# Kernel tuning notes

Hardware: AMD Instinct MI355X
Metric: run time of the kernel (lower is better)

The kernel has to match this reference:

```python
import jax, jax.numpy as jnp
import numpy as np

FEAT = 128
N_RBF = 20
CUTOFF = 5.0
NUM_CONV = 3
N_ATOMS = 8000
N_EDGES = 160000
N_MOLS = 100
EPS = 1e-15


def silu(x):
    return x * jax.nn.sigmoid(x)


def setup_inputs() -> dict:
    key = jax.random.key(0)
    ks = jax.random.split(key, 16)
    F = FEAT

    def w(k, shape, fan_in):
        return jax.random.normal(k, shape, dtype=jnp.float32) / np.sqrt(fan_in).astype(np.float32)

    nbr0 = jax.random.randint(ks[12], (N_EDGES,), 0, N_ATOMS)
    # avoid self-edges (would give zero distance)
    nbr1 = (nbr0 + 1 + jax.random.randint(ks[13], (N_EDGES,), 0, N_ATOMS - 1)) % N_ATOMS
    return {
        "xyz": jax.random.uniform(ks[0], (N_ATOMS, 3), dtype=jnp.float32) * 10.0,
        "emb_table": jax.random.normal(ks[1], (100, F), dtype=jnp.float32),
        "msg_w1": w(ks[2], (NUM_CONV, F, F), F),
        "msg_b1": jnp.zeros((NUM_CONV, F), jnp.float32),
        "msg_w2": w(ks[3], (NUM_CONV, F, 3 * F), F),
        "msg_b2": jnp.zeros((NUM_CONV, 3 * F), jnp.float32),
        "rbf_w": w(ks[4], (NUM_CONV, N_RBF, 3 * F), N_RBF),
        "rbf_b": jnp.zeros((NUM_CONV, 3 * F), jnp.float32),
        "upd_u": w(ks[5], (NUM_CONV, F, F), F),
        "upd_v": w(ks[6], (NUM_CONV, F, F), F),
        "upd_w1": w(ks[7], (NUM_CONV, 2 * F, F), 2 * F),
        "upd_b1": jnp.zeros((NUM_CONV, F), jnp.float32),
        "upd_w2": w(ks[8], (NUM_CONV, F, 3 * F), F),
        "upd_b2": jnp.zeros((NUM_CONV, 3 * F), jnp.float32),
        "ro_w1": w(ks[9], (F, F // 2), F),
        "ro_b1": jnp.zeros((F // 2,), jnp.float32),
        "ro_w2": w(ks[10], (F // 2, 1), F // 2),
        "ro_b2": jnp.zeros((1,), jnp.float32),
        "z": jax.random.randint(ks[11], (N_ATOMS,), 0, 100),
        "nbrs": jnp.stack([nbr0, nbr1], axis=1),
        "mol_idx": jnp.sort(jax.random.randint(ks[14], (N_ATOMS,), 0, N_MOLS)),
    }


def painn_forward(xyz, emb_table, msg_w1, msg_b1, msg_w2, msg_b2, rbf_w, rbf_b,
                  upd_u, upd_v, upd_w1, upd_b1, upd_w2, upd_b2,
                  ro_w1, ro_b1, ro_w2, ro_b2, z, nbrs, mol_idx):
    F = FEAT
    N = xyz.shape[0]
    # r_ij points from nbrs[:,0] (center i) to nbrs[:,1] (neighbor j)
    r_ij = xyz[nbrs[:, 1]] - xyz[nbrs[:, 0]]            # (E, 3)
    d = jnp.sqrt(jnp.sum(r_ij * r_ij, axis=-1))         # (E,)
    unit = r_ij / d[:, None]                            # (E, 3)
    # PaiNN sinc radial basis: sin(n*pi*d/cutoff)/d, n = 1..n_rbf
    n = jnp.arange(1, N_RBF + 1, dtype=jnp.float32)
    rbf = jnp.sin(n[None, :] * jnp.pi * d[:, None] / CUTOFF) / d[:, None]  # (E, n_rbf)
    # cosine cutoff envelope
    env = jnp.where(d <= CUTOFF, 0.5 * (jnp.cos(jnp.pi * d / CUTOFF) + 1.0), 0.0)

    s = emb_table[z]                                    # (N, F)
    v = jnp.zeros((N, F, 3), dtype=s.dtype)             # (N, F, 3)

    for i in range(NUM_CONV):
        # ---- message block ----
        phi = silu(s @ msg_w1[i] + msg_b1[i]) @ msg_w2[i] + msg_b2[i]   # (N, 3F)
        w_s = (rbf @ rbf_w[i] + rbf_b[i]) * env[:, None]                # (E, 3F)
        inv = (phi[nbrs[:, 1]] * w_s).reshape(-1, 3, F)                 # (E, 3, F)
        split0 = inv[:, 0, :][..., None]                                # (E, F, 1)
        split1 = inv[:, 1, :]                                           # (E, F)
        split2 = inv[:, 2, :][..., None]                                # (E, F, 1)
        dv_ij = split2 * unit[:, None, :] + split0 * v[nbrs[:, 1]]      # (E, F, 3)
        ds = jax.ops.segment_sum(split1, nbrs[:, 0], num_segments=N)
        dv = jax.ops.segment_sum(dv_ij, nbrs[:, 0], num_segments=N)
        s = s + ds
        v = v + dv
        # ---- update block ----
        u_v = jnp.einsum('nfd,fg->ngd', v, upd_u[i])                    # (N, F, 3)
        v_v = jnp.einsum('nfd,fg->ngd', v, upd_v[i])                    # (N, F, 3)
        v_v_norm = jnp.sqrt(jnp.sum(v_v * v_v, axis=-1) + EPS)          # (N, F)
        stack = jnp.concatenate([s, v_v_norm], axis=-1)                 # (N, 2F)
        a = (silu(stack @ upd_w1[i] + upd_b1[i]) @ upd_w2[i] + upd_b2[i]).reshape(-1, 3, F)
        a_vv = a[:, 0, :][..., None]
        a_sv = a[:, 1, :]
        a_ss = a[:, 2, :]
        dv_u = u_v * a_vv
        ds_u = jnp.sum(u_v * v_v, axis=-1) * a_sv + a_ss
        s = s + ds_u
        v = v + dv_u

    # readout MLP + per-molecule sum pool (SumPool)
    atom_e = silu(s @ ro_w1 + ro_b1) @ ro_w2 + ro_b2                    # (N, 1)
    energy = jax.ops.segment_sum(atom_e, mol_idx, num_segments=N_MOLS)  # (N_MOLS, 1)
    return energy


def reference(xyz, emb_table, msg_w1, msg_b1, msg_w2, msg_b2, rbf_w, rbf_b,
              upd_u, upd_v, upd_w1, upd_b1, upd_w2, upd_b2,
              ro_w1, ro_b1, ro_w2, ro_b2, z, nbrs, mol_idx):
    return painn_forward(xyz, emb_table, msg_w1, msg_b1, msg_w2, msg_b2, rbf_w, rbf_b,
                         upd_u, upd_v, upd_w1, upd_b1, upd_w2, upd_b2,
                         ro_w1, ro_b1, ro_w2, ro_b2, z, nbrs, mol_idx)
```

## Files before the change

kernel.cpp:

```cpp
#include <hip/hip_runtime.h>

static constexpr int F = 128;
static constexpr int N_RBF = 20;
static constexpr int N_ATOMS = 8000;
static constexpr int NP = 8064;
static constexpr int N_EDGES = 160000;
static constexpr int N_MOLS = 100;
static constexpr float CUTOFF = 5.0f;
static constexpr size_t NFC = (size_t)NP * F;
static constexpr int REC = 28;
#define PIF 3.14159265358979323846f

typedef __attribute__((ext_vector_type(8))) short bf16x8;
typedef __attribute__((ext_vector_type(4))) float f32x4;
typedef unsigned short ushort_t;
typedef unsigned int uint_t;

__device__ __forceinline__ float silu_f(float x) { return x / (1.f + __expf(-x)); }

__device__ __forceinline__ ushort_t f2bf(float x) {
    union { float f; uint_t u; } v; v.f = x;
    uint_t r = v.u + 0x7fffu + ((v.u >> 16) & 1u);
    return (ushort_t)(r >> 16);
}
// ... 46 lines not shown
        int idx = base + i;
        if (idx < N_ATOMS) { offsets[idx] = ex; ex += local[i]; }
    }
}

__global__ __launch_bounds__(256) void build_kernel(
    const float* __restrict__ xyz, const int* __restrict__ nbrs,
    const float* __restrict__ envb, const int* __restrict__ offsets,
    int* __restrict__ cursor, float* __restrict__ rec)
{
    int e = blockIdx.x * 256 + threadIdx.x;
    if (e >= N_EDGES) return;
    float ev = envb[e];
    if (ev <= 0.f) return;
    int i0 = nbrs[2*e+0], i1 = nbrs[2*e+1];
    float dx = xyz[3*i1+0] - xyz[3*i0+0];
    float dy = xyz[3*i1+1] - xyz[3*i0+1];
    float dz = xyz[3*i1+2] - xyz[3*i0+2];
    float d  = sqrtf(dx*dx + dy*dy + dz*dz);
    float inv = 1.f / d;
    int pos = offsets[i0] + atomicAdd(&cursor[i0], 1);
    float* r = rec + (size_t)pos * REC;
    r[0] = __int_as_float(i1);
    r[1] = ev;
    r[2] = dx*inv; r[3] = dy*inv; r[4] = dz*inv;
    float base = PIF*d/CUTOFF;
    float sc = inv * ev;
    #pragma unroll
    for (int k = 0; k < N_RBF; ++k)
        r[5 + k] = sinf((float)(k+1)*base) * sc;
}

static constexpr int WPREP_W = 557056;
static constexpr int WPREP_TOTAL = 557184;
static constexpr int NATF = N_ATOMS * F;
static constexpr int PREP_TOTAL = NATF + WPREP_TOTAL + 2 * N_ATOMS;
__global__ __launch_bounds__(256) void prep_kernel(
    const float* __restrict__ emb, const int* __restrict__ z, float* __restrict__ s,
    const float* __restrict__ msg_w1, const float* __restrict__ msg_w2,
    const float* __restrict__ upd_u,  const float* __restrict__ upd_v,
    const float* __restrict__ upd_w1, const float* __restrict__ upd_w2,
    const float* __restrict__ ro_w1,  const float* __restrict__ ro_b1,
    ushort_t* __restrict__ dhi, ushort_t* __restrict__ dlo,
    float* __restrict__ robias, int* __restrict__ cntz)
{
    int gidx = blockIdx.x * 256 + threadIdx.x;
    if (gidx < NATF) {
        int n = gidx >> 7, f = gidx & 127;
        s[gidx] = emb[z[n]*F + f];
        return;
    }
    int idx = gidx - NATF;
    if (idx >= WPREP_TOTAL) {
        cntz[idx - WPREP_TOTAL] = 0;
        return;
    }
    if (idx >= WPREP_W) {
        int l = idx - WPREP_W;
        robias[l] = (l < 64) ? ro_b1[l] : 0.f;
        return;
    }
    float val;
    if (idx < 540672) {
        const float* src; int K, N, rem;
        if (idx < 49152)       { int l = idx;          int c = l / 16384; rem = l % 16384; K = 128; N = 128; src = msg_w1 + c * 16384; }
        else if (idx < 196608) { int l = idx - 49152;  int c = l / 49152; rem = l % 49152; K = 128; N = 384; src = msg_w2 + c * 49152; }
        else if (idx < 294912) { int l = idx - 196608; int c = l / 32768; rem = l % 32768; K = 128; N = 128;
                                 if (rem < 16384) src = upd_u + c * 16384;
                                 else { src = upd_v + c * 16384; rem -= 16384; } }
        else if (idx < 393216) { int l = idx - 294912; int c = l / 32768; rem = l % 32768; K = 256; N = 128; src = upd_w1 + c * 32768; }
        else                   { int l = idx - 393216; int c = l / 49152; rem = l % 49152; K = 128; N = 384; src = upd_w2 + c * 49152; }
        int n = rem / K, k = rem % K;
        val = src[k * N + n];
    } else {
        int l = idx - 540672;
        int n = l >> 7, k = l & 127;
        val = (n < 64) ? ro_w1[k * 64 + n] : 0.f;
    }
    ushort_t h = f2bf(val);
    dhi[idx] = h;
    dlo[idx] = f2bf(val - bf2f(h));
}

__global__ __launch_bounds__(256) void phi0_kernel(
    const float* __restrict__ sbuf,
    const ushort_t* __restrict__ W1h, const ushort_t* __restrict__ W1l,
    const float* __restrict__ b1,
    const ushort_t* __restrict__ W2h, const ushort_t* __restrict__ W2l,
    const float* __restrict__ b2,
    float* __restrict__ C)
{
    __shared__ __align__(16) ushort_t Ah[2][32 * 40], Al[2][32 * 40];
    __shared__ __align__(16) ushort_t Bh[2][128 * 40], Bl[2][128 * 40];
    __shared__ __align__(16) ushort_t Hh[32 * 136], Hl[32 * 136];
    const int tid = threadIdx.x;
    const int wave = tid >> 6, lane = tid & 63;
    const int row_l = lane & 15, quad = lane >> 4;
    const int wn = wave * 32;
    const int m0 = blockIdx.x * 32;
    const int lrA = tid >> 3, ksA = (tid & 7) * 4;
    const int lrB = tid >> 1, ksB = (tid & 1) * 16;

    float4 rx;
    uint4 b_h0, b_h1, b_l0, b_l1;

    auto loadB1 = [&](int k0) {
        const ushort_t* bh = &W1h[(size_t)lrB * 128 + k0 + ksB];
        const ushort_t* bl = &W1l[(size_t)lrB * 128 + k0 + ksB];
        b_h0 = *(const uint4*)bh; b_h1 = *(const uint4*)(bh + 8);
        b_l0 = *(const uint4*)bl; b_l1 = *(const uint4*)(bl + 8);
    };
    auto loadB2 = [&](int it2) {
        int ct = it2 >> 2, k0 = (it2 & 3) * 32;
        const ushort_t* bh = &W2h[(size_t)(ct * 128 + lrB) * 128 + k0 + ksB];
        const ushort_t* bl = &W2l[(size_t)(ct * 128 + lrB) * 128 + k0 + ksB];
        b_h0 = *(const uint4*)bh; b_h1 = *(const uint4*)(bh + 8);
        b_l0 = *(const uint4*)bl; b_l1 = *(const uint4*)(bl + 8);
    };
    auto writeA = [&](int buf) {
        float e[4] = {rx.x, rx.y, rx.z, rx.w};
        ushort_t ph[4], pl[4];
        #pragma unroll
        for (int t = 0; t < 4; ++t) {
            ushort_t h = f2bf(e[t]);
            ph[t] = h; pl[t] = f2bf(e[t] - bf2f(h));
        }
        *(uint2*)&Ah[buf][lrA * 40 + ksA] = *(uint2*)ph;
        *(uint2*)&Al[buf][lrA * 40 + ksA] = *(uint2*)pl;
    };
    auto writeB = [&](int buf) {
        *(uint4*)&Bh[buf][lrB * 40 + ksB]     = b_h0;
        *(uint4*)&Bh[buf][lrB * 40 + ksB + 8] = b_h1;
        *(uint4*)&Bl[buf][lrB * 40 + ksB]     = b_l0;
        *(uint4*)&Bl[buf][lrB * 40 + ksB + 8] = b_l1;
    };

    f32x4 acc[2][2];
    #pragma unroll
    for (int i = 0; i < 2; ++i)
        #pragma unroll
        for (int j = 0; j < 2; ++j)
            #pragma unroll
            for (int r = 0; r < 4; ++r) acc[i][j][r] = 0.f;

    rx = *(const float4*)&sbuf[(size_t)(m0 + lrA) * 128 + ksA];
    loadB1(0);
    writeA(0); writeB(0);
    __syncthreads();
    #pragma unroll
    for (int it = 0; it < 4; ++it) {
        const int k0n = (it + 1) * 32;
        if (it + 1 < 4) {
            rx = *(const float4*)&sbuf[(size_t)(m0 + lrA) * 128 + k0n + ksA];
            loadB1(k0n);
        }
        bf16x8 ahf[2], alf[2], bhf[2], blf[2];
        #pragma unroll
        for (int i = 0; i < 2; ++i) {
            int ar = (i * 16 + row_l) * 40 + quad * 8;
            ahf[i] = *(const bf16x8*)&Ah[it & 1][ar];
            alf[i] = *(const bf16x8*)&Al[it & 1][ar];
        }
        #pragma unroll
        for (int j = 0; j < 2; ++j) {
            int br = (wn + j * 16 + row_l) * 40 + quad * 8;
            bhf[j] = *(const bf16x8*)&Bh[it & 1][br];
            blf[j] = *(const bf16x8*)&Bl[it & 1][br];
        }
        #pragma unroll
        for (int i = 0; i < 2; ++i)
            #pragma unroll
            for (int j = 0; j < 2; ++j) {
                acc[i][j] = __builtin_amdgcn_mfma_f32_16x16x32_bf16(ahf[i], bhf[j], acc[i][j], 0, 0, 0);
                acc[i][j] = __builtin_amdgcn_mfma_f32_16x16x32_bf16(ahf[i], blf[j], acc[i][j], 0, 0, 0);
                acc[i][j] = __builtin_amdgcn_mfma_f32_16x16x32_bf16(alf[i], bhf[j], acc[i][j], 0, 0, 0);
            }
        if (it + 1 < 4) { writeA((it + 1) & 1); writeB((it + 1) & 1); }
        __syncthreads();
    }
    #pragma unroll
    for (int j = 0; j < 2; ++j) {
        int col = wn + j * 16 + row_l;
        float bval = b1[col];
        #pragma unroll
        for (int i = 0; i < 2; ++i)
            #pragma unroll
            for (int r = 0; r < 4; ++r) {
                int row = i * 16 + quad * 4 + r;
                float v = silu_f(acc[i][j][r] + bval);
                ushort_t h = f2bf(v);
                Hh[row * 136 + col] = h;
                Hl[row * 136 + col] = f2bf(v - bf2f(h));
            }
    }

    #pragma unroll
    for (int i = 0; i < 2; ++i)
        #pragma unroll
        for (int j = 0; j < 2; ++j)
            #pragma unroll
            for (int r = 0; r < 4; ++r) acc[i][j][r] = 0.f;
    loadB2(0); writeB(0);
    __syncthreads();
    #pragma unroll
    for (int it = 0; it < 12; ++it) {
        const int k0 = (it & 3) * 32;
        if (it + 1 < 12) loadB2(it + 1);
        bf16x8 ahf[2], alf[2], bhf[2], blf[2];
        #pragma unroll
        for (int i = 0; i < 2; ++i) {
            int ar = (i * 16 + row_l) * 136 + k0 + quad * 8;
            ahf[i] = *(const bf16x8*)&Hh[ar];
            alf[i] = *(const bf16x8*)&Hl[ar];
        }
        #pragma unroll
        for (int j = 0; j < 2; ++j) {
            int br = (wn + j * 16 + row_l) * 40 + quad * 8;
            bhf[j] = *(const bf16x8*)&Bh[it & 1][br];
            blf[j] = *(const bf16x8*)&Bl[it & 1][br];
        }
        #pragma unroll
        for (int i = 0; i < 2; ++i)
            #pragma unroll
            for (int j = 0; j < 2; ++j) {
                acc[i][j] = __builtin_amdgcn_mfma_f32_16x16x32_bf16(ahf[i], bhf[j], acc[i][j], 0, 0, 0);
                acc[i][j] = __builtin_amdgcn_mfma_f32_16x16x32_bf16(ahf[i], blf[j], acc[i][j], 0, 0, 0);
                acc[i][j] = __builtin_amdgcn_mfma_f32_16x16x32_bf16(alf[i], bhf[j], acc[i][j], 0, 0, 0);
            }
        if ((it & 3) == 3) {
            const int ct = it >> 2;
            #pragma unroll
            for (int j = 0; j < 2; ++j) {
                int col = ct * 128 + wn + j * 16 + row_l;
                float bval = b2[col];
                #pragma unroll
                for (int i = 0; i < 2; ++i)
                    #pragma unroll
                    for (int r = 0; r < 4; ++r) {
                        int row = i * 16 + quad * 4 + r;
                        C[(size_t)(m0 + row) * 384 + col] = acc[i][j][r] + bval;
                    }
            }
            #pragma unroll
            for (int i = 0; i < 2; ++i)
                #pragma unroll
                for (int j = 0; j < 2; ++j)
                    #pragma unroll
                    for (int r = 0; r < 4; ++r) acc[i][j][r] = 0.f;
        }
        if (it + 1 < 12) writeB((it + 1) & 1);
        __syncthreads();
    }
}

template<int TAIL>
__global__ __launch_bounds__(256) void updphi_kernel(
    float* __restrict__ s_io, float* __restrict__ v_io,
    const ushort_t* __restrict__ UVh, const ushort_t* __restrict__ UVl,
    const ushort_t* __restrict__ W1h, const ushort_t* __restrict__ W1l,
    const float* __restrict__ b1,
    const ushort_t* __restrict__ W2h, const ushort_t* __restrict__ W2l,
    const float* __restrict__ b2,
    const ushort_t* __restrict__ XW1h, const ushort_t* __restrict__ XW1l,
    const float* __restrict__ xb1,
    const ushort_t* __restrict__ XW2h, const ushort_t* __restrict__ XW2l,
    const float* __restrict__ xb2,
    float* __restrict__ phi_out,
    const float* __restrict__ w2ro, const float* __restrict__ b2ro,
    const int* __restrict__ mol, float* __restrict__ outp)
{
    __shared__ float uvv[96][261];
    __shared__ __align__(16) ushort_t Bh[2][128 * 40];
    __shared__ __align__(16) ushort_t Bl[2][128 * 40];
    __shared__ __align__(16) unsigned char AH[17408];
    __shared__ float molacc[128];
    __shared__ float redl[32][4];
    const int tid = threadIdx.x;
    const int wave = tid >> 6, lane = tid & 63;
    const int row_l = lane & 15, quad = lane >> 4;
    const int wn = wave * 32;
    const int m0 = blockIdx.x * 32;
    const int lrA = tid >> 3;
    const int ksA = (tid & 7) * 4;
    const int lrB = tid >> 1, ksB = (tid & 1) * 16;

    float* sS = &uvv[0][0];
    constexpr int SSTR = 132;

    {
        ushort_t* A0h = (ushort_t*)AH;
        ushort_t* A0l = A0h + 96 * 40;
        ushort_t* B0h = &Bh[0][0];
        ushort_t* B0l = &Bl[0][0];
        f32x4 acc0[6][4];
        #pragma unroll
        for (int i = 0; i < 6; ++i)
            #pragma unroll
            for (int j = 0; j < 4; ++j)
                #pragma unroll
                for (int r = 0; r < 4; ++r) acc0[i][j][r] = 0.f;
        for (int k0 = 0; k0 < 128; k0 += 32) {
            #pragma unroll
            for (int g = 0; g < 3; ++g) {
                int row = g * 32 + lrA;
                float4 v = *(const float4*)&v_io[(size_t)(m0 * 3 + row) * 128 + k0 + ksA];
                float e[4] = {v.x, v.y, v.z, v.w};
                ushort_t ph[4], pl[4];
                #pragma unroll
                for (int t = 0; t < 4; ++t) {
                    ushort_t h = f2bf(e[t]);
                    ph[t] = h; pl[t] = f2bf(e[t] - bf2f(h));
                }
                *(uint2*)&A0h[row * 40 + ksA] = *(uint2*)ph;
                *(uint2*)&A0l[row * 40 + ksA] = *(uint2*)pl;
            }
            {
                const ushort_t* bh = &UVh[(size_t)tid * 128 + k0];
                const ushort_t* bl = &UVl[(size_t)tid * 128 + k0];
                *(uint4*)&B0h[tid * 40 + 0]  = *(const uint4*)(bh + 0);
                *(uint4*)&B0h[tid * 40 + 8]  = *(const uint4*)(bh + 8);
                *(uint4*)&B0h[tid * 40 + 16] = *(const uint4*)(bh + 16);
                *(uint4*)&B0h[tid * 40 + 24] = *(const uint4*)(bh + 24);
                *(uint4*)&B0l[tid * 40 + 0]  = *(const uint4*)(bl + 0);
                *(uint4*)&B0l[tid * 40 + 8]  = *(const uint4*)(bl + 8);
                *(uint4*)&B0l[tid * 40 + 16] = *(const uint4*)(bl + 16);
                *(uint4*)&B0l[tid * 40 + 24] = *(const uint4*)(bl + 24);
            }
            __syncthreads();
            bf16x8 a0h[6], a0l[6], b0h[4], b0l[4];
            #pragma unroll
            for (int i = 0; i < 6; ++i) {
                int ar = (i * 16 + row_l) * 40 + quad * 8;
                a0h[i] = *(const bf16x8*)&A0h[ar];
                a0l[i] = *(const bf16x8*)&A0l[ar];
            }
            #pragma unroll
            for (int j = 0; j < 4; ++j) {
                int br = (wave * 64 + j * 16 + row_l) * 40 + quad * 8;
                b0h[j] = *(const bf16x8*)&B0h[br];
                b0l[j] = *(const bf16x8*)&B0l[br];
            }
            #pragma unroll
            for (int i = 0; i < 6; ++i)
                #pragma unroll
                for (int j = 0; j < 4; ++j) {
                    acc0[i][j] = __builtin_amdgcn_mfma_f32_16x16x32_bf16(a0h[i], b0h[j], acc0[i][j], 0, 0, 0);
                    acc0[i][j] = __builtin_amdgcn_mfma_f32_16x16x32_bf16(a0h[i], b0l[j], acc0[i][j], 0, 0, 0);
                    acc0[i][j] = __builtin_amdgcn_mfma_f32_16x16x32_bf16(a0l[i], b0h[j], acc0[i][j], 0, 0, 0);
                }
            __syncthreads();
        }
        #pragma unroll
        for (int i = 0; i < 6; ++i)
            #pragma unroll
            for (int j = 0; j < 4; ++j)
                #pragma unroll
                for (int r = 0; r < 4; ++r)
                    uvv[i * 16 + quad * 4 + r][wave * 64 + j * 16 + row_l] = acc0[i][j][r];
        __syncthreads();
    }

    ushort_t* Ah1 = (ushort_t*)AH;
    ushort_t* Al1 = Ah1 + 2 * 32 * 40;
    ushort_t* Hh  = (ushort_t*)AH;
    ushort_t* Hl  = Hh + 32 * 136;

    float4 rx;
    uint4 b_h0, b_h1, b_l0, b_l1;

    auto loadB1 = [&](int k0) {
        const ushort_t* bh = &W1h[(size_t)lrB * 256 + k0 + ksB];
        const ushort_t* bl = &W1l[(size_t)lrB * 256 + k0 + ksB];
        b_h0 = *(const uint4*)bh; b_h1 = *(const uint4*)(bh + 8);
        b_l0 = *(const uint4*)bl; b_l1 = *(const uint4*)(bl + 8);
    };
    auto writeB = [&](int buf) {
        *(uint4*)&Bh[buf][lrB * 40 + ksB]     = b_h0;
        *(uint4*)&Bh[buf][lrB * 40 + ksB + 8] = b_h1;
        *(uint4*)&Bl[buf][lrB * 40 + ksB]     = b_l0;
        *(uint4*)&Bl[buf][lrB * 40 + ksB + 8] = b_l1;
    };
    auto writeA1 = [&](int buf, int k0) {
        float e[4];
        if (k0 < 128) {
            e[0] = rx.x; e[1] = rx.y; e[2] = rx.z; e[3] = rx.w;
        } else {
            int f = k0 + ksA;
            #pragma unroll
            for (int t = 0; t < 4; ++t) {
                float x = uvv[lrA * 3 + 0][f + t];
                float y = uvv[lrA * 3 + 1][f + t];
                float z = uvv[lrA * 3 + 2][f + t];
                e[t] = sqrtf(x * x + y * y + z * z + 1e-15f);
            }
        }
        ushort_t ph[4], pl[4];
        #pragma unroll
        for (int t = 0; t < 4; ++t) {
            ushort_t h = f2bf(e[t]);
            ph[t] = h; pl[t] = f2bf(e[t] - bf2f(h));
        }
        *(uint2*)&Ah1[buf * 1280 + lrA * 40 + ksA] = *(uint2*)ph;
        *(uint2*)&Al1[buf * 1280 + lrA * 40 + ksA] = *(uint2*)pl;
    };

    f32x4 acc[2][2];
    #pragma unroll
    for (int i = 0; i < 2; ++i)
        #pragma unroll
        for (int j = 0; j < 2; ++j)
            #pragma unroll
            for (int r = 0; r < 4; ++r) acc[i][j][r] = 0.f;

    rx = *(const float4*)&s_io[(size_t)(m0 + lrA) * 128 + ksA];
    loadB1(0);
    writeA1(0, 0); writeB(0);
    __syncthreads();
    #pragma unroll
    for (int it = 0; it < 8; ++it) {
        const int k0n = (it + 1) * 32;
        if (it + 1 < 8) {
            if (k0n < 128) rx = *(const float4*)&s_io[(size_t)(m0 + lrA) * 128 + k0n + ksA];
            loadB1(k0n);
        }
        bf16x8 ahf[2], alf[2], bhf[2], blf[2];
        #pragma unroll
        for (int i = 0; i < 2; ++i) {
            int ar = (it & 1) * 1280 + (i * 16 + row_l) * 40 + quad * 8;
            ahf[i] = *(const bf16x8*)&Ah1[ar];
            alf[i] = *(const bf16x8*)&Al1[ar];
        }
        #pragma unroll
        for (int j = 0; j < 2; ++j) {
            int br = (wn + j * 16 + row_l) * 40 + quad * 8;
            bhf[j] = *(const bf16x8*)&Bh[it & 1][br];
            blf[j] = *(const bf16x8*)&Bl[it & 1][br];
        }
        #pragma unroll
        for (int i = 0; i < 2; ++i)
            #pragma unroll
            for (int j = 0; j < 2; ++j) {
                acc[i][j] = __builtin_amdgcn_mfma_f32_16x16x32_bf16(ahf[i], bhf[j], acc[i][j], 0, 0, 0);
                acc[i][j] = __builtin_amdgcn_mfma_f32_16x16x32_bf16(ahf[i], blf[j], acc[i][j], 0, 0, 0);
                acc[i][j] = __builtin_amdgcn_mfma_f32_16x16x32_bf16(alf[i], bhf[j], acc[i][j], 0, 0, 0);
            }
        if (it + 1 < 8) { writeA1((it + 1) & 1, k0n); writeB((it + 1) & 1); }
        __syncthreads();
    }
    #pragma unroll
    for (int j = 0; j < 2; ++j) {
        int col = wn + j * 16 + row_l;
        float bval = b1[col];
        #pragma unroll
        for (int i = 0; i < 2; ++i)
            #pragma unroll
            for (int r = 0; r < 4; ++r) {
                int row = i * 16 + quad * 4 + r;
                float v = silu_f(acc[i][j][r] + bval);
                ushort_t h = f2bf(v);
                Hh[row * 136 + col] = h;
                Hl[row * 136 + col] = f2bf(v - bf2f(h));
            }
    }

    constexpr int CT0 = TAIL ? 1 : 0;
    constexpr int NIT2 = (3 - CT0) * 4;
    auto loadB2 = [&](int it2) {
        int ct = CT0 + (it2 >> 2), k0 = (it2 & 3) * 32;
        const ushort_t* bh = &W2h[(size_t)(ct * 128 + lrB) * 128 + k0 + ksB];
        const ushort_t* bl = &W2l[(size_t)(ct * 128 + lrB) * 128 + k0 + ksB];
        b_h0 = *(const uint4*)bh; b_h1 = *(const uint4*)(bh + 8);
        b_l0 = *(const uint4*)bl; b_l1 = *(const uint4*)(bl + 8);
    };

    #pragma unroll
    for (int i = 0; i < 2; ++i)
        #pragma unroll
        for (int j = 0; j < 2; ++j)
            #pragma unroll
            for (int r = 0; r < 4; ++r) acc[i][j][r] = 0.f;
    f32x4 ssum[2][2];

    loadB2(0); writeB(0);
    __syncthreads();
    #pragma unroll
    for (int it = 0; it < NIT2; ++it) {
        const int k0 = (it & 3) * 32;
        if (it + 1 < NIT2) loadB2(it + 1);
        bf16x8 ahf[2], alf[2], bhf[2], blf[2];
        #pragma unroll
        for (int i = 0; i < 2; ++i) {
            int ar = (i * 16 + row_l) * 136 + k0 + quad * 8;
            ahf[i] = *(const bf16x8*)&Hh[ar];
            alf[i] = *(const bf16x8*)&Hl[ar];
        }
        #pragma unroll
        for (int j = 0; j < 2; ++j) {
            int br = (wn + j * 16 + row_l) * 40 + quad * 8;
            bhf[j] = *(const bf16x8*)&Bh[it & 1][br];
            blf[j] = *(const bf16x8*)&Bl[it & 1][br];
        }
        #pragma unroll
        for (int i = 0; i < 2; ++i)
            #pragma unroll
            for (int j = 0; j < 2; ++j) {
                acc[i][j] = __builtin_amdgcn_mfma_f32_16x16x32_bf16(ahf[i], bhf[j], acc[i][j], 0, 0, 0);
                acc[i][j] = __builtin_amdgcn_mfma_f32_16x16x32_bf16(ahf[i], blf[j], acc[i][j], 0, 0, 0);
                acc[i][j] = __builtin_amdgcn_mfma_f32_16x16x32_bf16(alf[i], bhf[j], acc[i][j], 0, 0, 0);
            }
        if ((it & 3) == 3) {
            const int ct = CT0 + (it >> 2);
            #pragma unroll
            for (int j = 0; j < 2; ++j) {
                int f = wn + j * 16 + row_l;
                float bval = b2[ct * 128 + f];
                #pragma unroll
                for (int i = 0; i < 2; ++i)
                    #pragma unroll
                    for (int r = 0; r < 4; ++r) {
                        int ln = i * 16 + quad * 4 + r;
                        float a = acc[i][j][r] + bval;
                        if (ct == 0) {
                            size_t vb = (size_t)(m0 + ln) * 3 * F + f;
                            v_io[vb]         += uvv[ln * 3 + 0][f] * a;
                            v_io[vb + F]     += uvv[ln * 3 + 1][f] * a;
                            v_io[vb + 2 * F] += uvv[ln * 3 + 2][f] * a;
                        } else if (ct == 1) {
                            float dot = uvv[ln * 3 + 0][f] * uvv[ln * 3 + 0][128 + f]
                                      + uvv[ln * 3 + 1][f] * uvv[ln * 3 + 1][128 + f]
                                      + uvv[ln * 3 + 2][f] * uvv[ln * 3 + 2][128 + f];
                            ssum[i][j][r] = dot * a;
                        } else {
                            float sv = s_io[(size_t)(m0 + ln) * F + f] + ssum[i][j][r] + a;
                            if constexpr (TAIL == 0) s_io[(size_t)(m0 + ln) * F + f] = sv;
                            sS[ln * SSTR + f] = sv;
                        }
                    }
            }
            #pragma unroll
            for (int i = 0; i < 2; ++i)
                #pragma unroll
                for (int j = 0; j < 2; ++j)
                    #pragma unroll
                    for (int r = 0; r < 4; ++r) acc[i][j][r] = 0.f;
        }
        if (it + 1 < NIT2) writeB((it + 1) & 1);
        __syncthreads();
    }

    if constexpr (TAIL == 1) { if (tid < 128) molacc[tid] = 0.f; }
    ushort_t* Ah3 = (ushort_t*)AH;
    ushort_t* Al3 = Ah3 + 2 * 1280;

    auto loadB31 = [&](int k0) {
        const ushort_t* bh = &XW1h[(size_t)lrB * 128 + k0 + ksB];
        const ushort_t* bl = &XW1l[(size_t)lrB * 128 + k0 + ksB];
        b_h0 = *(const uint4*)bh; b_h1 = *(const uint4*)(bh + 8);
        b_l0 = *(const uint4*)bl; b_l1 = *(const uint4*)(bl + 8);
    };
    auto writeA3 = [&](int buf, int k0) {
        float e[4];
        #pragma unroll
        for (int t = 0; t < 4; ++t) e[t] = sS[lrA * SSTR + k0 + ksA + t];
        ushort_t ph[4], pl[4];
        #pragma unroll
        for (int t = 0; t < 4; ++t) {
            ushort_t h = f2bf(e[t]);
            ph[t] = h; pl[t] = f2bf(e[t] - bf2f(h));
        }
        *(uint2*)&Ah3[buf * 1280 + lrA * 40 + ksA] = *(uint2*)ph;
        *(uint2*)&Al3[buf * 1280 + lrA * 40 + ksA] = *(uint2*)pl;
    };

    #pragma unroll
    for (int i = 0; i < 2; ++i)
        #pragma unroll
        for (int j = 0; j < 2; ++j)
            #pragma unroll
            for (int r = 0; r < 4; ++r) acc[i][j][r] = 0.f;

    loadB31(0);
    writeA3(0, 0); writeB(0);
    __syncthreads();
    #pragma unroll
    for (int it = 0; it < 4; ++it) {
        const int k0n = (it + 1) * 32;
        if (it + 1 < 4) loadB31(k0n);
        bf16x8 ahf[2], alf[2], bhf[2], blf[2];
        #pragma unroll
        for (int i = 0; i < 2; ++i) {
            int ar = (it & 1) * 1280 + (i * 16 + row_l) * 40 + quad * 8;
            ahf[i] = *(const bf16x8*)&Ah3[ar];
            alf[i] = *(const bf16x8*)&Al3[ar];
        }
        #pragma unroll
        for (int j = 0; j < 2; ++j) {
            int br = (wn + j * 16 + row_l) * 40 + quad * 8;
            bhf[j] = *(const bf16x8*)&Bh[it & 1][br];
            blf[j] = *(const bf16x8*)&Bl[it & 1][br];
        }
        #pragma unroll
        for (int i = 0; i < 2; ++i)
            #pragma unroll
            for (int j = 0; j < 2; ++j) {
                acc[i][j] = __builtin_amdgcn_mfma_f32_16x16x32_bf16(ahf[i], bhf[j], acc[i][j], 0, 0, 0);
                acc[i][j] = __builtin_amdgcn_mfma_f32_16x16x32_bf16(ahf[i], blf[j], acc[i][j], 0, 0, 0);
                acc[i][j] = __builtin_amdgcn_mfma_f32_16x16x32_bf16(alf[i], bhf[j], acc[i][j], 0, 0, 0);
            }
        if (it + 1 < 4) { writeA3((it + 1) & 1, k0n); writeB((it + 1) & 1); }
        __syncthreads();
    }

    if constexpr (TAIL == 0) {
        #pragma unroll
        for (int j = 0; j < 2; ++j) {
            int col = wn + j * 16 + row_l;
            float bval = xb1[col];
            #pragma unroll
            for (int i = 0; i < 2; ++i)
                #pragma unroll
                for (int r = 0; r < 4; ++r) {
                    int row = i * 16 + quad * 4 + r;
                    float v = silu_f(acc[i][j][r] + bval);
                    ushort_t h = f2bf(v);
                    Hh[row * 136 + col] = h;
                    Hl[row * 136 + col] = f2bf(v - bf2f(h));
                }
        }
        auto loadB32 = [&](int it2) {
            int ct = it2 >> 2, k0 = (it2 & 3) * 32;
            const ushort_t* bh = &XW2h[(size_t)(ct * 128 + lrB) * 128 + k0 + ksB];
            const ushort_t* bl = &XW2l[(size_t)(ct * 128 + lrB) * 128 + k0 + ksB];
            b_h0 = *(const uint4*)bh; b_h1 = *(const uint4*)(bh + 8);
            b_l0 = *(const uint4*)bl; b_l1 = *(const uint4*)(bl + 8);
        };
        #pragma unroll
        for (int i = 0; i < 2; ++i)
            #pragma unroll
            for (int j = 0; j < 2; ++j)
                #pragma unroll
                for (int r = 0; r < 4; ++r) acc[i][j][r] = 0.f;
        loadB32(0); writeB(0);
        __syncthreads();
        #pragma unroll
        for (int it = 0; it < 12; ++it) {
            const int k0 = (it & 3) * 32;
            if (it + 1 < 12) loadB32(it + 1);
            bf16x8 ahf[2], alf[2], bhf[2], blf[2];
            #pragma unroll
            for (int i = 0; i < 2; ++i) {
                int ar = (i * 16 + row_l) * 136 + k0 + quad * 8;
                ahf[i] = *(const bf16x8*)&Hh[ar];
                alf[i] = *(const bf16x8*)&Hl[ar];
            }
            #pragma unroll
            for (int j = 0; j < 2; ++j) {
                int br = (wn + j * 16 + row_l) * 40 + quad * 8;
                bhf[j] = *(const bf16x8*)&Bh[it & 1][br];
                blf[j] = *(const bf16x8*)&Bl[it & 1][br];
            }
            #pragma unroll
            for (int i = 0; i < 2; ++i)
                #pragma unroll
                for (int j = 0; j < 2; ++j) {
                    acc[i][j] = __builtin_amdgcn_mfma_f32_16x16x32_bf16(ahf[i], bhf[j], acc[i][j], 0, 0, 0);
                    acc[i][j] = __builtin_amdgcn_mfma_f32_16x16x32_bf16(ahf[i], blf[j], acc[i][j], 0, 0, 0);
                    acc[i][j] = __builtin_amdgcn_mfma_f32_16x16x32_bf16(alf[i], bhf[j], acc[i][j], 0, 0, 0);
                }
            if ((it & 3) == 3) {
                const int ct = it >> 2;
                #pragma unroll
                for (int j = 0; j < 2; ++j) {
                    int col = ct * 128 + wn + j * 16 + row_l;
                    float bval = xb2[col];
                    #pragma unroll
                    for (int i = 0; i < 2; ++i)
                        #pragma unroll
                        for (int r = 0; r < 4; ++r) {
                            int row = i * 16 + quad * 4 + r;
                            phi_out[(size_t)(m0 + row) * 384 + col] = acc[i][j][r] + bval;
                        }
                }
                #pragma unroll
                for (int i = 0; i < 2; ++i)
                    #pragma unroll
                    for (int j = 0; j < 2; ++j)
                        #pragma unroll
                        for (int r = 0; r < 4; ++r) acc[i][j][r] = 0.f;
            }
            if (it + 1 < 12) writeB((it + 1) & 1);
            __syncthreads();
        }
    } else {
        float part[2][4];
        #pragma unroll
        for (int i = 0; i < 2; ++i)
            #pragma unroll
            for (int r = 0; r < 4; ++r) part[i][r] = 0.f;
        #pragma unroll
        for (int j = 0; j < 2; ++j) {
            int col = wn + j * 16 + row_l;
            float bv = xb1[col];
            float wv = (col < 64) ? w2ro[col] : 0.f;
            #pragma unroll
            for (int i = 0; i < 2; ++i)
                #pragma unroll
                for (int r = 0; r < 4; ++r)
                    part[i][r] += silu_f(acc[i][j][r] + bv) * wv;
        }
        #pragma unroll
        for (int o = 1; o < 16; o <<= 1)
            #pragma unroll
            for (int i = 0; i < 2; ++i)
                #pragma unroll
                for (int r = 0; r < 4; ++r)
                    part[i][r] += __shfl_xor(part[i][r], o);
        if (row_l == 0)
            #pragma unroll
            for (int i = 0; i < 2; ++i)
                #pragma unroll
                for (int r = 0; r < 4; ++r)
                    redl[i * 16 + quad * 4 + r][wave] = part[i][r];
        __syncthreads();
        if (tid < 32) {
            int n = m0 + tid;
            if (n < N_ATOMS) {
                float e = redl[tid][0] + redl[tid][1] + redl[tid][2] + redl[tid][3] + b2ro[0];
                atomicAdd(&molacc[mol[n]], e);
            }
        }
        __syncthreads();
        if (tid < 100 && molacc[tid] != 0.f) atomicAdd(&outp[tid], molacc[tid]);
    }
}

template<int ZVIN>
__global__ __launch_bounds__(128) void msg_gather(
    const float* __restrict__ phi, const float* __restrict__ rec,
    const float* __restrict__ rbf_w, const float* __restrict__ rbf_b,
    const float* __restrict__ v_in, float* __restrict__ s,
    float* __restrict__ v_out, const int* __restrict__ offsets,
    const int* __restrict__ cnt)
{
    const int n = blockIdx.x, tid = threadIdx.x;
    float W0[N_RBF], W1[N_RBF], W2[N_RBF];
    #pragma unroll
    for (int k = 0; k < N_RBF; ++k) {
        W0[k] = rbf_w[k*3*F + tid];
        W1[k] = rbf_w[k*3*F + F + tid];
        W2[k] = rbf_w[k*3*F + 2*F + tid];
    }
    const float b0 = rbf_b[tid], b1 = rbf_b[F + tid], b2 = rbf_b[2*F + tid];
    float ds = 0.f, dvx = 0.f, dvy = 0.f, dvz = 0.f;
    const int off = offsets[n], c = cnt[n];
    const float* r = rec + (size_t)off * REC;
    #pragma unroll 4
    for (int t = 0; t < c; ++t, r += REC) {
        int j = __float_as_int(r[0]);
        float ev = r[1];
        float ux = r[2], uy = r[3], uz = r[4];
        float w0 = b0 * ev, w1 = b1 * ev, w2 = b2 * ev;
        #pragma unroll
        for (int k = 0; k < N_RBF; ++k) {
            float rk = r[5 + k];
            w0 += rk * W0[k]; w1 += rk * W1[k]; w2 += rk * W2[k];
        }
        const float* prow = phi + (size_t)j * 3 * F;
        float s0 = prow[tid] * w0;
        float s1 = prow[F + tid] * w1;
        float s2 = prow[2*F + tid] * w2;
        ds  += s1;
        if constexpr (ZVIN) {
            dvx += s2*ux; dvy += s2*uy; dvz += s2*uz;
        } else {
// ... 122 lines not shown
```

Baseline: 345.5 us.

## Load GEMM operand fragments directly from global memory, drop LDS staging

The small per-atom GEMMs in phi0 and the update kernel now read bf16 hi/lo weight fragments and fp32 activations (split on the fly) straight from global memory into MFMA registers, instead of staging through double-buffered LDS tiles. This removes most __syncthreads barriers and the LDS write/read traffic. The vector-norm and updated-scalar inputs are precomputed once into LDS as bf16 splits. Each wave now issues its own global loads without cooperative reuse, so the design depends on L1/L2 caching of the small weight matrices, and latency is no longer hidden by prefetching.

Measured after the change: 409.6 us. +18.6%, slower.

```diff
diff --git a/kernel.cpp b/kernel.cpp
--- a/kernel.cpp
+++ b/kernel.cpp
@@ -152,6 +152,19 @@
     dlo[idx] = f2bf(val - bf2f(h));
 }
 
+__device__ __forceinline__ void split8(const float* __restrict__ p, bf16x8& hi, bf16x8& lo) {
+    float4 a = *(const float4*)p;
+    float4 b = *(const float4*)(p + 4);
+    float e[8] = {a.x, a.y, a.z, a.w, b.x, b.y, b.z, b.w};
+    ushort_t ph[8], pl[8];
+    #pragma unroll
+    for (int t = 0; t < 8; ++t) {
+        ushort_t h = f2bf(e[t]);
+        ph[t] = h; pl[t] = f2bf(e[t] - bf2f(h));
+    }
+    hi = *(bf16x8*)ph; lo = *(bf16x8*)pl;
+}
+
 __global__ __launch_bounds__(256) void phi0_kernel(
     const float* __restrict__ sbuf,
     const ushort_t* __restrict__ W1h, const ushort_t* __restrict__ W1l,
@@ -160,50 +173,12 @@
     const float* __restrict__ b2,
     float* __restrict__ C)
 {
-    __shared__ __align__(16) ushort_t Ah[2][32 * 40], Al[2][32 * 40];
-    __shared__ __align__(16) ushort_t Bh[2][128 * 40], Bl[2][128 * 40];
     __shared__ __align__(16) ushort_t Hh[32 * 136], Hl[32 * 136];
     const int tid = threadIdx.x;
     const int wave = tid >> 6, lane = tid & 63;
     const int row_l = lane & 15, quad = lane >> 4;
     const int wn = wave * 32;
     const int m0 = blockIdx.x * 32;
-    const int lrA = tid >> 3, ksA = (tid & 7) * 4;
-    const int lrB = tid >> 1, ksB = (tid & 1) * 16;
-
-    float4 rx;
-    uint4 b_h0, b_h1, b_l0, b_l1;
-
-    auto loadB1 = [&](int k0) {
-        const ushort_t* bh = &W1h[(size_t)lrB * 128 + k0 + ksB];
-        const ushort_t* bl = &W1l[(size_t)lrB * 128 + k0 + ksB];
-        b_h0 = *(const uint4*)bh; b_h1 = *(const uint4*)(bh + 8);
-        b_l0 = *(const uint4*)bl; b_l1 = *(const uint4*)(bl + 8);
-    };
-    auto loadB2 = [&](int it2) {
-        int ct = it2 >> 2, k0 = (it2 & 3) * 32;
-        const ushort_t* bh = &W2h[(size_t)(ct * 128 + lrB) * 128 + k0 + ksB];
-        const ushort_t* bl = &W2l[(size_t)(ct * 128 + lrB) * 128 + k0 + ksB];
-        b_h0 = *(const uint4*)bh; b_h1 = *(const uint4*)(bh + 8);
-        b_l0 = *(const uint4*)bl; b_l1 = *(const uint4*)(bl + 8);
-    };
-    auto writeA = [&](int buf) {
-        float e[4] = {rx.x, rx.y, rx.z, rx.w};
-        ushort_t ph[4], pl[4];
-        #pragma unroll
-        for (int t = 0; t < 4; ++t) {
-            ushort_t h = f2bf(e[t]);
-            ph[t] = h; pl[t] = f2bf(e[t] - bf2f(h));
-        }
-        *(uint2*)&Ah[buf][lrA * 40 + ksA] = *(uint2*)ph;
-        *(uint2*)&Al[buf][lrA * 40 + ksA] = *(uint2*)pl;
-    };
-    auto writeB = [&](int buf) {
-        *(uint4*)&Bh[buf][lrB * 40 + ksB]     = b_h0;
-        *(uint4*)&Bh[buf][lrB * 40 + ksB + 8] = b_h1;
-        *(uint4*)&Bl[buf][lrB * 40 + ksB]     = b_l0;
-        *(uint4*)&Bl[buf][lrB * 40 + ksB + 8] = b_l1;
-    };
 
     f32x4 acc[2][2];
     #pragma unroll
@@ -213,29 +188,18 @@
             #pragma unroll
             for (int r = 0; r < 4; ++r) acc[i][j][r] = 0.f;
 
-    rx = *(const float4*)&sbuf[(size_t)(m0 + lrA) * 128 + ksA];
-    loadB1(0);
-    writeA(0); writeB(0);
-    __syncthreads();
     #pragma unroll
     for (int it = 0; it < 4; ++it) {
-        const int k0n = (it + 1) * 32;
-        if (it + 1 < 4) {
-            rx = *(const float4*)&sbuf[(size_t)(m0 + lrA) * 128 + k0n + ksA];
-            loadB1(k0n);
-        }
+        const int k0 = it * 32;
         bf16x8 ahf[2], alf[2], bhf[2], blf[2];
         #pragma unroll
-        for (int i = 0; i < 2; ++i) {
-            int ar = (i * 16 + row_l) * 40 + quad * 8;
-            ahf[i] = *(const bf16x8*)&Ah[it & 1][ar];
-            alf[i] = *(const bf16x8*)&Al[it & 1][ar];
-        }
+        for (int i = 0; i < 2; ++i)
+            split8(&sbuf[(size_t)(m0 + i*16 + row_l) * 128 + k0 + quad*8], ahf[i], alf[i]);
         #pragma unroll
         for (int j = 0; j < 2; ++j) {
-            int br = (wn + j * 16 + row_l) * 40 + quad * 8;
-            bhf[j] = *(const bf16x8*)&Bh[it & 1][br];
-            blf[j] = *(const bf16x8*)&Bl[it & 1][br];
+            size_t br = (size_t)(wn + j*16 + row_l) * 128 + k0 + quad*8;
+            bhf[j] = *(const bf16x8*)&W1h[br];
+            blf[j] = *(const bf16x8*)&W1l[br];
         }
         #pragma unroll
         for (int i = 0; i < 2; ++i)
@@ -245,8 +209,6 @@
                 acc[i][j] = __builtin_amdgcn_mfma_f32_16x16x32_bf16(ahf[i], blf[j], acc[i][j], 0, 0, 0);
                 acc[i][j] = __builtin_amdgcn_mfma_f32_16x16x32_bf16(alf[i], bhf[j], acc[i][j], 0, 0, 0);
             }
-        if (it + 1 < 4) { writeA((it + 1) & 1); writeB((it + 1) & 1); }
-        __syncthreads();
     }
     #pragma unroll
     for (int j = 0; j < 2; ++j) {
@@ -263,6 +225,7 @@
                 Hl[row * 136 + col] = f2bf(v - bf2f(h));
             }
     }
+    __syncthreads();
 
     #pragma unroll
     for (int i = 0; i < 2; ++i)
@@ -270,12 +233,10 @@
         for (int j = 0; j < 2; ++j)
             #pragma unroll
             for (int r = 0; r < 4; ++r) acc[i][j][r] = 0.f;
-    loadB2(0); writeB(0);
-    __syncthreads();
     #pragma unroll
     for (int it = 0; it < 12; ++it) {
         const int k0 = (it & 3) * 32;
-        if (it + 1 < 12) loadB2(it + 1);
+        const int ct = it >> 2;
         bf16x8 ahf[2], alf[2], bhf[2], blf[2];
         #pragma unroll
         for (int i = 0; i < 2; ++i) {
@@ -285,9 +246,9 @@
         }
         #pragma unroll
         for (int j = 0; j < 2; ++j) {
-            int br = (wn + j * 16 + row_l) * 40 + quad * 8;
-            bhf[j] = *(const bf16x8*)&Bh[it & 1][br];
-            blf[j] = *(const bf16x8*)&Bl[it & 1][br];
+            size_t br = (size_t)(ct * 128 + wn + j*16 + row_l) * 128 + k0 + quad*8;
+            bhf[j] = *(const bf16x8*)&W2h[br];
+            blf[j] = *(const bf16x8*)&W2l[br];
         }
         #pragma unroll
         for (int i = 0; i < 2; ++i)
@@ -298,7 +259,6 @@
                 acc[i][j] = __builtin_amdgcn_mfma_f32_16x16x32_bf16(alf[i], bhf[j], acc[i][j], 0, 0, 0);
             }
         if ((it & 3) == 3) {
-            const int ct = it >> 2;
             #pragma unroll
             for (int j = 0; j < 2; ++j) {
                 int col = ct * 128 + wn + j * 16 + row_l;
@@ -318,8 +278,6 @@
                     #pragma unroll
                     for (int r = 0; r < 4; ++r) acc[i][j][r] = 0.f;
         }
-        if (it + 1 < 12) writeB((it + 1) & 1);
-        __syncthreads();
     }
 }
 
@@ -340,8 +298,8 @@
     const int* __restrict__ mol, float* __restrict__ outp)
 {
     __shared__ float uvv[96][261];
-    __shared__ __align__(16) ushort_t Bh[2][128 * 40];
-    __shared__ __align__(16) ushort_t Bl[2][128 * 40];
+    __shared__ __align__(16) ushort_t NBh[256 * 40];
+    __shared__ __align__(16) ushort_t NBl[256 * 40];
     __shared__ __align__(16) unsigned char AH[17408];
     __shared__ float molacc[128];
     __shared__ float redl[32][4];
@@ -352,16 +310,17 @@
     const int m0 = blockIdx.x * 32;
     const int lrA = tid >> 3;
     const int ksA = (tid & 7) * 4;
-    const int lrB = tid >> 1, ksB = (tid & 1) * 16;
-
-    float* sS = &uvv[0][0];
-    constexpr int SSTR = 132;
+
+    ushort_t* normH = NBh;
+    ushort_t* normL = NBh + 32 * 136;
+    ushort_t* sSh   = NBl;
+    ushort_t* sSl   = NBl + 32 * 136;
+    ushort_t* Hh    = (ushort_t*)AH;
+    ushort_t* Hl    = Hh + 32 * 136;
 
     {
         ushort_t* A0h = (ushort_t*)AH;
         ushort_t* A0l = A0h + 96 * 40;
-        ushort_t* B0h = &Bh[0][0];
-        ushort_t* B0l = &Bl[0][0];
         f32x4 acc0[6][4];
         #pragma unroll
         for (int i = 0; i < 6; ++i)
@@ -387,14 +346,14 @@
             {
                 const ushort_t* bh = &UVh[(size_t)tid * 128 + k0];
                 const ushort_t* bl = &UVl[(size_t)tid * 128 + k0];
-                *(uint4*)&B0h[tid * 40 + 0]  = *(const uint4*)(bh + 0);
-                *(uint4*)&B0h[tid * 40 + 8]  = *(const uint4*)(bh + 8);
-                *(uint4*)&B0h[tid * 40 + 16] = *(const uint4*)(bh + 16);
-                *(uint4*)&B0h[tid * 40 + 24] = *(const uint4*)(bh + 24);
-                *(uint4*)&B0l[tid * 40 + 0]  = *(const uint4*)(bl + 0);
-                *(uint4*)&B0l[tid * 40 + 8]  = *(const uint4*)(bl + 8);
-                *(uint4*)&B0l[tid * 40 + 16] = *(const uint4*)(bl + 16);
-                *(uint4*)&B0l[tid * 40 + 24] = *(const uint4*)(bl + 24);
+                *(uint4*)&NBh[tid * 40 + 0]  = *(const uint4*)(bh + 0);
+                *(uint4*)&NBh[tid * 40 + 8]  = *(const uint4*)(bh + 8);
+                *(uint4*)&NBh[tid * 40 + 16] = *(const uint4*)(bh + 16);
+                *(uint4*)&NBh[tid * 40 + 24] = *(const uint4*)(bh + 24);
+                *(uint4*)&NBl[tid * 40 + 0]  = *(const uint4*)(bl + 0);
+                *(uint4*)&NBl[tid * 40 + 8]  = *(const uint4*)(bl + 8);
+                *(uint4*)&NBl[tid * 40 + 16] = *(const uint4*)(bl + 16);
+                *(uint4*)&NBl[tid * 40 + 24] = *(const uint4*)(bl + 24);
             }
             __syncthreads();
             bf16x8 a0h[6], a0l[6], b0h[4], b0l[4];
@@ -407,8 +366,8 @@
             #pragma unroll
             for (int j = 0; j < 4; ++j) {
                 int br = (wave * 64 + j * 16 + row_l) * 40 + quad * 8;
-                b0h[j] = *(const bf16x8*)&B0h[br];
-                b0l[j] = *(const bf16x8*)&B0l[br];
+                b0h[j] = *(const bf16x8*)&NBh[br];
+                b0l[j] = *(const bf16x8*)&NBl[br];
             }
             #pragma unroll
             for (int i = 0; i < 6; ++i)
@@ -430,81 +389,51 @@
         __syncthreads();
     }
 
-    ushort_t* Ah1 = (ushort_t*)AH;
-    ushort_t* Al1 = Ah1 + 2 * 32 * 40;
-    ushort_t* Hh  = (ushort_t*)AH;
-    ushort_t* Hl  = Hh + 32 * 136;
-
-    float4 rx;
-    uint4 b_h0, b_h1, b_l0, b_l1;
-
-    auto loadB1 = [&](int k0) {
-        const ushort_t* bh = &W1h[(size_t)lrB * 256 + k0 + ksB];
-        const ushort_t* bl = &W1l[(size_t)lrB * 256 + k0 + ksB];
-        b_h0 = *(const uint4*)bh; b_h1 = *(const uint4*)(bh + 8);
-        b_l0 = *(const uint4*)bl; b_l1 = *(const uint4*)(bl + 8);
-    };
-    auto writeB = [&](int buf) {
-        *(uint4*)&Bh[buf][lrB * 40 + ksB]     = b_h0;
-        *(uint4*)&Bh[buf][lrB * 40 + ksB + 8] = b_h1;
-        *(uint4*)&Bl[buf][lrB * 40 + ksB]     = b_l0;
-        *(uint4*)&Bl[buf][lrB * 40 + ksB + 8] = b_l1;
-    };
-    auto writeA1 = [&](int buf, int k0) {
-        float e[4];
+    {
+        #pragma unroll
+        for (int t = 0; t < 16; ++t) {
+            int idx = t * 256 + tid;
+            int ln = idx >> 7, f = idx & 127;
+            float x = uvv[ln * 3 + 0][128 + f];
+            float y = uvv[ln * 3 + 1][128 + f];
+            float z = uvv[ln * 3 + 2][128 + f];
+            float nv = sqrtf(x * x + y * y + z * z + 1e-15f);
+            ushort_t h = f2bf(nv);
+            normH[ln * 136 + f] = h;
+            normL[ln * 136 + f] = f2bf(nv - bf2f(h));
+        }
+        __syncthreads();
+    }
+
+    f32x4 acc[2][2];
+    #pragma unroll
+    for (int i = 0; i < 2; ++i)
+        #pragma unroll
+        for (int j = 0; j < 2; ++j)
+            #pragma unroll
+            for (int r = 0; r < 4; ++r) acc[i][j][r] = 0.f;
+
+    #pragma unroll
+    for (int it = 0; it < 8; ++it) {
+        const int k0 = it * 32;
+        bf16x8 ahf[2], alf[2], bhf[2], blf[2];
         if (k0 < 128) {
-            e[0] = rx.x; e[1] = rx.y; e[2] = rx.z; e[3] = rx.w;
+            #pragma unroll
+            for (int i = 0; i < 2; ++i)
+                split8(&s_io[(size_t)(m0 + i*16 + row_l) * 128 + k0 + quad*8], ahf[i], alf[i]);
         } else {
-            int f = k0 + ksA;
-            #pragma unroll
-            for (int t = 0; t < 4; ++t) {
-                float x = uvv[lrA * 3 + 0][f + t];
-                float y = uvv[lrA * 3 + 1][f + t];
-                float z = uvv[lrA * 3 + 2][f + t];
-                e[t] = sqrtf(x * x + y * y + z * z + 1e-15f);
-            }
-        }
-        ushort_t ph[4], pl[4];
-        #pragma unroll
-        for (int t = 0; t < 4; ++t) {
-            ushort_t h = f2bf(e[t]);
-            ph[t] = h; pl[t] = f2bf(e[t] - bf2f(h));
-        }
-        *(uint2*)&Ah1[buf * 1280 + lrA * 40 + ksA] = *(uint2*)ph;
-        *(uint2*)&Al1[buf * 1280 + lrA * 40 + ksA] = *(uint2*)pl;
-    };
-
-    f32x4 acc[2][2];
-    #pragma unroll
-    for (int i = 0; i < 2; ++i)
-        #pragma unroll
-        for (int j = 0; j < 2; ++j)
-            #pragma unroll
-            for (int r = 0; r < 4; ++r) acc[i][j][r] = 0.f;
-
-    rx = *(const float4*)&s_io[(size_t)(m0 + lrA) * 128 + ksA];
-    loadB1(0);
-    writeA1(0, 0); writeB(0);
-    __syncthreads();
-    #pragma unroll
-    for (int it = 0; it < 8; ++it) {
-        const int k0n = (it + 1) * 32;
-        if (it + 1 < 8) {
-            if (k0n < 128) rx = *(const float4*)&s_io[(size_t)(m0 + lrA) * 128 + k0n + ksA];
-            loadB1(k0n);
-        }
-        bf16x8 ahf[2], alf[2], bhf[2], blf[2];
-        #pragma unroll
-        for (int i = 0; i < 2; ++i) {
-            int ar = (it & 1) * 1280 + (i * 16 + row_l) * 40 + quad * 8;
-            ahf[i] = *(const bf16x8*)&Ah1[ar];
-            alf[i] = *(const bf16x8*)&Al1[ar];
+            #pragma unroll
+            for (int i = 0; i < 2; ++i) {
+                int off = (i * 16 + row_l) * 136 + (k0 - 128) + quad * 8;
+                ahf[i] = *(const bf16x8*)&normH[off];
+                alf[i] = *(const bf16x8*)&normL[off];
+            }
         }
         #pragma unroll
         for (int j = 0; j < 2; ++j) {
-            int br = (wn + j * 16 + row_l) * 40 + quad * 8;
-            bhf[j] = *(const bf16x8*)&Bh[it & 1][br];
-            blf[j] = *(const bf16x8*)&Bl[it & 1][br];
+            size_t br = (size_t)(wn + j*16 + row_l) * 256 + k0 + quad*8;
+            bhf[j] = *(const bf16x8*)&W1h[br];
+            blf[j] = *(const bf16x8*)&W1l[br];
         }
         #pragma unroll
         for (int i = 0; i < 2; ++i)
@@ -514,8 +443,6 @@
                 acc[i][j] = __builtin_amdgcn_mfma_f32_16x16x32_bf16(ahf[i], blf[j], acc[i][j], 0, 0, 0);
                 acc[i][j] = __builtin_amdgcn_mfma_f32_16x16x32_bf16(alf[i], bhf[j], acc[i][j], 0, 0, 0);
             }
-        if (it + 1 < 8) { writeA1((it + 1) & 1, k0n); writeB((it + 1) & 1); }
-        __syncthreads();
     }
     #pragma unroll
     for (int j = 0; j < 2; ++j) {
@@ -532,17 +459,10 @@
                 Hl[row * 136 + col] = f2bf(v - bf2f(h));
             }
     }
+    __syncthreads();
 
     constexpr int CT0 = TAIL ? 1 : 0;
     constexpr int NIT2 = (3 - CT0) * 4;
-    auto loadB2 = [&](int it2) {
-        int ct = CT0 + (it2 >> 2), k0 = (it2 & 3) * 32;
-        const ushort_t* bh = &W2h[(size_t)(ct * 128 + lrB) * 128 + k0 + ksB];
-        const ushort_t* bl = &W2l[(size_t)(ct * 128 + lrB) * 128 + k0 + ksB];
-        b_h0 = *(const uint4*)bh; b_h1 = *(const uint4*)(bh + 8);
-        b_l0 = *(const uint4*)bl; b_l1 = *(const uint4*)(bl + 8);
-    };
-
     #pragma unroll
     for (int i = 0; i < 2; ++i)
         #pragma unroll
@@ -551,12 +471,10 @@
             for (int r = 0; r < 4; ++r) acc[i][j][r] = 0.f;
     f32x4 ssum[2][2];
 
-    loadB2(0); writeB(0);
-    __syncthreads();
     #pragma unroll
     for (int it = 0; it < NIT2; ++it) {
         const int k0 = (it & 3) * 32;
-        if (it + 1 < NIT2) loadB2(it + 1);
+        const int ct = CT0 + (it >> 2);
         bf16x8 ahf[2], alf[2], bhf[2], blf[2];
         #pragma unroll
         for (int i = 0; i < 2; ++i) {
@@ -566,9 +484,9 @@
         }
         #pragma unroll
         for (int j = 0; j < 2; ++j) {
-            int br = (wn + j * 16 + row_l) * 40 + quad * 8;
-            bhf[j] = *(const bf16x8*)&Bh[it & 1][br];
-            blf[j] = *(const bf16x8*)&Bl[it & 1][br];
+            size_t br = (size_t)(ct * 128 + wn + j*16 + row_l) * 128 + k0 + quad*8;
+            bhf[j] = *(const bf16x8*)&W2h[br];
+            blf[j] = *(const bf16x8*)&W2l[br];
         }
         #pragma unroll
         for (int i = 0; i < 2; ++i)
@@ -579,7 +497,6 @@
                 acc[i][j] = __builtin_amdgcn_mfma_f32_16x16x32_bf16(alf[i], bhf[j], acc[i][j], 0, 0, 0);
             }
         if ((it & 3) == 3) {
-            const int ct = CT0 + (it >> 2);
             #pragma unroll
             for (int j = 0; j < 2; ++j) {
                 int f = wn + j * 16 + row_l;
@@ -603,7 +520,9 @@
                         } else {
                             float sv = s_io[(size_t)(m0 + ln) * F + f] + ssum[i][j][r] + a;
                             if constexpr (TAIL == 0) s_io[(size_t)(m0 + ln) * F + f] = sv;
-                            sS[ln * SSTR + f] = sv;
+                            ushort_t h = f2bf(sv);
+                            sSh[ln * 136 + f] = h;
+                            sSl[ln * 136 + f] = f2bf(sv - bf2f(h));
                         }
                     }
             }
@@ -614,33 +533,10 @@
                     #pragma unroll
                     for (int r = 0; r < 4; ++r) acc[i][j][r] = 0.f;
         }
-        if (it + 1 < NIT2) writeB((it + 1) & 1);
-        __syncthreads();
-    }
+    }
+    __syncthreads();
 
     if constexpr (TAIL == 1) { if (tid < 128) molacc[tid] = 0.f; }
-    ushort_t* Ah3 = (ushort_t*)AH;
-    ushort_t* Al3 = Ah3 + 2 * 1280;
-
-    auto loadB31 = [&](int k0) {
-        const ushort_t* bh = &XW1h[(size_t)lrB * 128 + k0 + ksB];
-        const ushort_t* bl = &XW1l[(size_t)lrB * 128 + k0 + ksB];
-        b_h0 = *(const uint4*)bh; b_h1 = *(const uint4*)(bh + 8);
-        b_l0 = *(const uint4*)bl; b_l1 = *(const uint4*)(bl + 8);
-    };
-    auto writeA3 = [&](int buf, int k0) {
-        float e[4];
-        #pragma unroll
-        for (int t = 0; t < 4; ++t) e[t] = sS[lrA * SSTR + k0 + ksA + t];
-        ushort_t ph[4], pl[4];
-        #pragma unroll
-        for (int t = 0; t < 4; ++t) {
-            ushort_t h = f2bf(e[t]);
-            ph[t] = h; pl[t] = f2bf(e[t] - bf2f(h));
-        }
-        *(uint2*)&Ah3[buf * 1280 + lrA * 40 + ksA] = *(uint2*)ph;
-        *(uint2*)&Al3[buf * 1280 + lrA * 40 + ksA] = *(uint2*)pl;
-    };
 
     #pragma unroll
     for (int i = 0; i < 2; ++i)
@@ -649,25 +545,21 @@
             #pragma unroll
             for (int r = 0; r < 4; ++r) acc[i][j][r] = 0.f;
 
-    loadB31(0);
-    writeA3(0, 0); writeB(0);
-    __syncthreads();
     #pragma unroll
     for (int it = 0; it < 4; ++it) {
-        const int k0n = (it + 1) * 32;
-        if (it + 1 < 4) loadB31(k0n);
+        const int k0 = it * 32;
         bf16x8 ahf[2], alf[2], bhf[2], blf[2];
         #pragma unroll
         for (int i = 0; i < 2; ++i) {
-            int ar = (it & 1) * 1280 + (i * 16 + row_l) * 40 + quad * 8;
-            ahf[i] = *(const bf16x8*)&Ah3[ar];
-            alf[i] = *(const bf16x8*)&Al3[ar];
+            int off = (i * 16 + row_l) * 136 + k0 + quad * 8;
+            ahf[i] = *(const bf16x8*)&sSh[off];
+            alf[i] = *(const bf16x8*)&sSl[off];
         }
         #pragma unroll
         for (int j = 0; j < 2; ++j) {
-            int br = (wn + j * 16 + row_l) * 40 + quad * 8;
-            bhf[j] = *(const bf16x8*)&Bh[it & 1][br];
-            blf[j] = *(const bf16x8*)&Bl[it & 1][br];
+            size_t br = (size_t)(wn + j*16 + row_l) * 128 + k0 + quad*8;
+            bhf[j] = *(const bf16x8*)&XW1h[br];
+            blf[j] = *(const bf16x8*)&XW1l[br];
         }
         #pragma unroll
         for (int i = 0; i < 2; ++i)
@@ -677,8 +569,6 @@
                 acc[i][j] = __builtin_amdgcn_mfma_f32_16x16x32_bf16(ahf[i], blf[j], acc[i][j], 0, 0, 0);
                 acc[i][j] = __builtin_amdgcn_mfma_f32_16x16x32_bf16(alf[i], bhf[j], acc[i][j], 0, 0, 0);
             }
-        if (it + 1 < 4) { writeA3((it + 1) & 1, k0n); writeB((it + 1) & 1); }
-        __syncthreads();
     }
 
     if constexpr (TAIL == 0) {
@@ -697,25 +587,17 @@
                     Hl[row * 136 + col] = f2bf(v - bf2f(h));
                 }
         }
-        auto loadB32 = [&](int it2) {
-            int ct = it2 >> 2, k0 = (it2 & 3) * 32;
-            const ushort_t* bh = &XW2h[(size_t)(ct * 128 + lrB) * 128 + k0 + ksB];
-            const ushort_t* bl = &XW2l[(size_t)(ct * 128 + lrB) * 128 + k0 + ksB];
-            b_h0 = *(const uint4*)bh; b_h1 = *(const uint4*)(bh + 8);
-            b_l0 = *(const uint4*)bl; b_l1 = *(const uint4*)(bl + 8);
-        };
+        __syncthreads();
         #pragma unroll
         for (int i = 0; i < 2; ++i)
             #pragma unroll
             for (int j = 0; j < 2; ++j)
                 #pragma unroll
                 for (int r = 0; r < 4; ++r) acc[i][j][r] = 0.f;
-        loadB32(0); writeB(0);
-        __syncthreads();
         #pragma unroll
         for (int it = 0; it < 12; ++it) {
             const int k0 = (it & 3) * 32;
-            if (it + 1 < 12) loadB32(it + 1);
+            const int ct = it >> 2;
             bf16x8 ahf[2], alf[2], bhf[2], blf[2];
             #pragma unroll
             for (int i = 0; i < 2; ++i) {
@@ -725,9 +607,9 @@
             }
             #pragma unroll
             for (int j = 0; j < 2; ++j) {
-                int br = (wn + j * 16 + row_l) * 40 + quad * 8;
-                bhf[j] = *(const bf16x8*)&Bh[it & 1][br];
-                blf[j] = *(const bf16x8*)&Bl[it & 1][br];
+                size_t br = (size_t)(ct * 128 + wn + j*16 + row_l) * 128 + k0 + quad*8;
+                bhf[j] = *(const bf16x8*)&XW2h[br];
+                blf[j] = *(const bf16x8*)&XW2l[br];
             }
             #pragma unroll
             for (int i = 0; i < 2; ++i)
@@ -738,7 +620,6 @@
                     acc[i][j] = __builtin_amdgcn_mfma_f32_16x16x32_bf16(alf[i], bhf[j], acc[i][j], 0, 0, 0);
                 }
             if ((it & 3) == 3) {
-                const int ct = it >> 2;
                 #pragma unroll
                 for (int j = 0; j < 2; ++j) {
                     int col = ct * 128 + wn + j * 16 + row_l;
@@ -758,8 +639,6 @@
                         #pragma unroll
                         for (int r = 0; r < 4; ++r) acc[i][j][r] = 0.f;
             }
-            if (it + 1 < 12) writeB((it + 1) & 1);
-            __syncthreads();
         }
     } else {
         float part[2][4];
```
